# Optimization experiments

Measured on AMD Instinct MI355X. Metric: run time of the kernel, lower is better.

## Reference

```python
import jax, jax.numpy as jnp
import numpy as np
from functools import reduce

N = 20          # total qubits
N_SQC = 4       # shadow-circuit qubits
REPEAT = 2      # BasicEntangleLayer repeat
CDTYPE = jnp.complex64

_I2 = jnp.eye(2, dtype=CDTYPE)
_X  = jnp.array([[0, 1], [1, 0]], dtype=CDTYPE)   # PauliX
_P0 = jnp.array([[1, 0], [0, 0]], dtype=CDTYPE)
_P1 = jnp.array([[0, 0], [0, 1]], dtype=CDTYPE)


def multi_kron(mats):
    return reduce(jnp.kron, mats)


def _ry(t):
    c = jnp.cos(t * 0.5).astype(CDTYPE)
    s = jnp.sin(t * 0.5).astype(CDTYPE)
    return jnp.stack([jnp.stack([c, -s]), jnp.stack([s, c])])


def _rz(t):
    e = jnp.exp(-0.5j * t.astype(CDTYPE))
    z = jnp.zeros((), CDTYPE)
    return jnp.stack([jnp.stack([e, z]), jnp.stack([z, jnp.conj(e)])])


def _yzy_layer(p, n):
    # per qubit i: Ry(p[3i]) then Rz(p[3i+1]) then Ry(p[3i+2])
    mats = [_ry(p[3 * i + 2]) @ _rz(p[3 * i + 1]) @ _ry(p[3 * i]) for i in range(n)]
    return multi_kron(mats)


def _cnot(c, t, n):
    a = [_I2] * n; a[c] = _P0
    b = [_I2] * n; b[c] = _P1; b[t] = _X
    return multi_kron(a) + multi_kron(b)


def _ring_of_cnot(n):
    U = jnp.eye(2 ** n, dtype=CDTYPE)
    for i in range(n):
        U = _cnot(i, (i + 1) % n, n) @ U
    return U


def build_circuit(weight):
    """BasicEntangleLayer (YZY rotations + ring of CNOTs, repeated) + final YZYLayer."""
    n = N_SQC
    ring = _ring_of_cnot(n)
    U = jnp.eye(2 ** n, dtype=CDTYPE)
    for r in range(REPEAT):
        p = weight[3 * n * r:3 * n * (r + 1)]
        U = ring @ (_yzy_layer(p, n) @ U)
    U = _yzy_layer(weight[3 * n * REPEAT:3 * n * (REPEAT + 1)], n) @ U
    return U


def setup_inputs() -> dict:
    key = jax.random.key(0)
    k1, k2 = jax.random.split(key)
    vector_batch = jax.random.normal(k1, (32, 2 ** N), dtype=jnp.float32)
    weight = jax.random.uniform(k2, (9 * N_SQC,), dtype=jnp.float32,
                                minval=0.0, maxval=2.0 * np.pi)
    return {"vector_batch": vector_batch, "weight": weight}


def reference(vector_batch, weight):
    B = vector_batch.shape[0]
    # row-wise L2 normalization, then amplitude encoding into 2^N complex state
    norm = jnp.linalg.norm(vector_batch, axis=1, keepdims=True)
    state = (vector_batch / jnp.maximum(norm, 1e-12)).astype(CDTYPE)  # (B, 2^N)

    U = build_circuit(weight)                        # (16, 16)
    M = multi_kron([_X] * N_SQC)                     # X^{\otimes n_sqc}
    temp = U.conj().T @ M @ U                        # (16, 16) Hermitian

    d = 2 ** N_SQC
    outs = []
    for q in range(N - N_SQC + 1):
        # apply temp locally on qubits [q, q+n_sqc): identical math to
        # <state| I^{\otimes q} (x) temp (x) I^{\otimes rest} |state>
        s = state.reshape(B, 2 ** q, d, -1)          # (B, left, 16, right)
        ts = jnp.einsum('ij,bajc->baic', temp, s)
        outs.append(jnp.einsum('bajc,bajc->b', s.conj(), ts).real)
    return jnp.stack(outs, axis=1).astype(jnp.float32)  # (B, N-n_sqc+1)
```

## Files before the change

kernel.cpp:

```cpp
#include <hip/hip_runtime.h>
#include <math.h>

#define WS_TU    0
#define WS_S     256
#define WS_N     800
#define WS_PART  1024
#define WS_NPART 35840
#define WS_NEED_BYTES ((WS_NPART + 2048) * 4)

typedef _Float16 half8 __attribute__((ext_vector_type(8)));
typedef float f32x4 __attribute__((ext_vector_type(4)));

__device__ inline float2 cmul2(float2 a, float2 b) {
  return make_float2(a.x * b.x - a.y * b.y, a.x * b.y + a.y * b.x);
}

__device__ inline int ringperm(int x) {
  if ((x >> 3) & 1) x ^= 4;
  if ((x >> 2) & 1) x ^= 2;
  if ((x >> 1) & 1) x ^= 1;
  if (x & 1)        x ^= 8;
  return x;
}

__device__ inline float2 yzy_elem(const float* wgt, int layer, int r, int c) {
  float2 prod = make_float2(1.f, 0.f);
#pragma unroll
  for (int k = 0; k < 4; k++) {
    float t0 = wgt[layer * 12 + 3 * k + 0];
    float t1 = wgt[layer * 12 + 3 * k + 1];
    float t2 = wgt[layer * 12 + 3 * k + 2];
    float s0, c0, s1, c1, s2, c2;
    sincosf(0.5f * t0, &s0, &c0);
    sincosf(0.5f * t1, &s1, &c1);
    sincosf(0.5f * t2, &s2, &c2);
    float A = c2 * c0, B = s2 * s0, C = c2 * s0, D = s2 * c0;
    float2 m00 = make_float2( c1 * (A - B), -s1 * (A + B));
    float2 m01 = make_float2(-c1 * (C + D),  s1 * (C - D));
    float2 m10 = make_float2( c1 * (C + D),  s1 * (C - D));
    float2 m11 = make_float2( c1 * (A - B),  s1 * (A + B));
    int rb = (r >> (3 - k)) & 1, cb = (c >> (3 - k)) & 1;
    float2 mm = rb ? (cb ? m11 : m10) : (cb ? m01 : m00);
    prod = cmul2(prod, mm);
  }
  return prod;
}

__global__ void build_T_kernel(const float* __restrict__ wgt, float* __restrict__ ws) {
  __shared__ float2 U[256], Y[256], W[256];
  const int t = threadIdx.x;
  const int r = t >> 4, c = t & 15;

  for (int k = t; k < 576; k += 256) ws[WS_S + k] = 0.f;

  U[t] = yzy_elem(wgt, 0, r, c);
  __syncthreads();
  W[ringperm(r) * 16 + c] = U[t];
  __syncthreads(); U[t] = W[t]; __syncthreads();
  Y[t] = yzy_elem(wgt, 1, r, c);
  __syncthreads();
  {
    float2 s = make_float2(0.f, 0.f);
#pragma unroll
    for (int k = 0; k < 16; k++) {
      float2 pr = cmul2(Y[r * 16 + k], U[k * 16 + c]);
      s.x += pr.x; s.y += pr.y;
    }
    W[t] = s;
  }
  __syncthreads(); U[t] = W[t]; __syncthreads();
  W[ringperm(r) * 16 + c] = U[t];
  __syncthreads(); U[t] = W[t]; __syncthreads();
  Y[t] = yzy_elem(wgt, 2, r, c);
  __syncthreads();
  {
    float2 s = make_float2(0.f, 0.f);
#pragma unroll
    for (int k = 0; k < 16; k++) {
      float2 pr = cmul2(Y[r * 16 + k], U[k * 16 + c]);
      s.x += pr.x; s.y += pr.y;
    }
    W[t] = s;
  }
  __syncthreads(); U[t] = W[t]; __syncthreads();
  Y[t] = U[(r ^ 15) * 16 + c];
  __syncthreads();
  float s_re = 0.f;
#pragma unroll
  for (int k = 0; k < 16; k++) {
    float2 u = U[k * 16 + r], m = Y[k * 16 + c];
    s_re += u.x * m.x + u.y * m.y;
  }
  ws[WS_TU + t] = s_re;
}

__device__ inline int swzB(int B) {
  int h = B >> 3;
  int f = (h ^ (h >> 3) ^ (h >> 6)) & 7;
  return B ^ f;
}

template <int P>
__device__ inline float windowM(const half8* __restrict__ HB, const float* __restrict__ Tr) {
  const int t = threadIdx.x;
  const int w = t >> 6, l = t & 63, g = l >> 4, i = l & 15;
  f32x4 hh[4] = {{0.f, 0.f, 0.f, 0.f}, {0.f, 0.f, 0.f, 0.f},
                 {0.f, 0.f, 0.f, 0.f}, {0.f, 0.f, 0.f, 0.f}};
#pragma unroll
  for (int s = 0; s < 2; s++) {
#pragma unroll
    for (int c = 0; c < 4; c++) {
      int rest = (w << 5) | ((s * 4 + c) << 2) | g;
      int rl = rest & ((1 << (P - 3)) - 1), rh = rest >> (P - 3);
      int pos = (rl << 3) | (i << P) | (rh << (P + 4));
      half8 fr = HB[swzB(pos >> 3)];
      hh[c] = __builtin_amdgcn_mfma_f32_16x16x32_f16(fr, fr, hh[c], 0, 0, 0);
    }
  }
  float part = 0.f;
#pragma unroll
  for (int reg = 0; reg < 4; reg++)
    part = fmaf(Tr[reg], (hh[0][reg] + hh[1][reg]) + (hh[2][reg] + hh[3][reg]), part);
  return part;
}

__global__ __launch_bounds__(256) void passAll_kernel(const float* __restrict__ vb,
                                                      float* ws, int use_part) {
  __shared__ half8 HB[2048];
  const int t = threadIdx.x;
  const int bid = blockIdx.x;

  const int mode = (bid < 2048) ? 0 : 2;
  const int idx = (bid < 2048) ? bid : bid - 2048;
  const int b = idx >> 6, chunk = idx & 63;
  const int l = t & 63, g = l >> 4, i = l & 15;

  float Treg[4];
#pragma unroll
  for (int reg = 0; reg < 4; reg++) Treg[reg] = ws[WS_TU + ((g * 4 + reg) << 4) + i];

  float nsum = 0.f;
  half8 h[8];
  if (mode == 0) {
    const float4* src4 = ((const float4*)vb) + ((size_t)b << 18) + ((size_t)chunk << 12);
#pragma unroll
    for (int j = 0; j < 8; j++) {
      int B = j * 256 + t;
      float4 a = src4[2 * B], c = src4[2 * B + 1];
      nsum = fmaf(a.x, a.x, nsum); nsum = fmaf(a.y, a.y, nsum);
      nsum = fmaf(a.z, a.z, nsum); nsum = fmaf(a.w, a.w, nsum);
      nsum = fmaf(c.x, c.x, nsum); nsum = fmaf(c.y, c.y, nsum);
      nsum = fmaf(c.z, c.z, nsum); nsum = fmaf(c.w, c.w, nsum);
      half8 hh;
      hh[0] = (_Float16)a.x; hh[1] = (_Float16)a.y; hh[2] = (_Float16)a.z; hh[3] = (_Float16)a.w;
      hh[4] = (_Float16)c.x; hh[5] = (_Float16)c.y; hh[6] = (_Float16)c.z; hh[7] = (_Float16)c.w;
      h[j] = hh;
      HB[swzB(B)] = hh;
    }
  } else {
    const float4* src4 = ((const float4*)vb) + ((size_t)b << 18) + chunk * 8;
#pragma unroll
    for (int j = 0; j < 8; j++) {
      int B = j * 256 + t;
      int row = B >> 2;
      int c4 = (B & 3) * 2;
      float4 a = src4[row * 512 + c4], c = src4[row * 512 + c4 + 1];
      half8 hh;
      hh[0] = (_Float16)a.x; hh[1] = (_Float16)a.y; hh[2] = (_Float16)a.z; hh[3] = (_Float16)a.w;
      hh[4] = (_Float16)c.x; hh[5] = (_Float16)c.y; hh[6] = (_Float16)c.z; hh[7] = (_Float16)c.w;
      HB[swzB(B)] = hh;
    }
  }
  __syncthreads();

  float part[11];
#pragma unroll
  for (int k = 0; k < 11; k++) part[k] = 0.f;

  int nwin;
#define DOWIN(P, WIN) part[WIN] = windowM<P>(HB, Treg);
  if (mode == 0) {
    nwin = 11;
    DOWIN(3, 0) DOWIN(4, 1) DOWIN(5, 2) DOWIN(6, 3)
    DOWIN(7, 4) DOWIN(8, 5) DOWIN(9, 6) DOWIN(10, 7)
    __syncthreads();
#pragma unroll
    for (int e = 0; e < 8; e++) {
      half8 v;
#pragma unroll
      for (int j = 0; j < 8; j++) v[j] = h[j][e];
      HB[swzB(8 * t + e)] = v;
    }
    __syncthreads();
    DOWIN(3, 8) DOWIN(4, 9) DOWIN(5, 10)
  } else {
    nwin = 6;
    DOWIN(5, 0) DOWIN(6, 1) DOWIN(7, 2)
    DOWIN(8, 3) DOWIN(9, 4) DOWIN(10, 5)
  }
#undef DOWIN
  __syncthreads();

  float* red2 = (float*)HB;
#pragma unroll
  for (int k = 0; k < 11; k++) red2[k * 256 + t] = part[k];
  red2[11 * 256 + t] = nsum;
  __syncthreads();

  const int win = t >> 4, idx16 = t & 15;
  const float4* r4 = (const float4*)red2;
  float4 q0 = r4[win * 64 + idx16],      q1 = r4[win * 64 + 16 + idx16];
  float4 q2 = r4[win * 64 + 32 + idx16], q3 = r4[win * 64 + 48 + idx16];
  float s1 = ((q0.x + q0.y) + (q0.z + q0.w)) + ((q1.x + q1.y) + (q1.z + q1.w)) +
             ((q2.x + q2.y) + (q2.z + q2.w)) + ((q3.x + q3.y) + (q3.z + q3.w));
#pragma unroll
  for (int off = 8; off; off >>= 1) s1 += __shfl_down(s1, off, 16);

  if (idx16 == 0) {
    if (mode == 0) {
      if (win < 11) {
        int q = (win < 8) ? (13 - win) : (24 - win);
        if (use_part) ws[WS_PART + (b * 17 + q) * 64 + chunk] = s1;
        else          atomicAdd(ws + WS_S + b * 17 + q, s1);
      } else if (win == 11) {
        if (use_part) ws[WS_NPART + b * 64 + chunk] = s1;
        else          atomicAdd(ws + WS_N + b, s1);
      }
    } else {
      if (win < 6) {
        int q = 5 - win;
        if (use_part) ws[WS_PART + (b * 17 + q) * 64 + chunk] = s1;
        else          atomicAdd(ws + WS_S + b * 17 + q, s1);
      }
    }
  }
}

__global__ void finalize_kernel(const float* __restrict__ ws, float* __restrict__ out,
                                int use_part) {
  int i = blockIdx.x * 256 + threadIdx.x;
  if (i < 544) {
    int b = i / 17;
    float s, n;
    if (use_part) {
      const float* sp = ws + WS_PART + i * 64;
      s = 0.f;
#pragma unroll 8
      for (int c = 0; c < 64; c++) s += sp[c];
      const float* np = ws + WS_NPART + b * 64;
      n = 0.f;
#pragma unroll 8
      for (int c = 0; c < 64; c++) n += np[c];
    } else {
      s = ws[WS_S + i];
      n = ws[WS_N + b];
    }
    out[i] = s / fmaxf(n, 1e-24f);
  }
}

extern "C" void kernel_launch(void* const* d_in, const int* in_sizes, int n_in,
                              void* d_out, int out_size, void* d_ws, size_t ws_size,
                              hipStream_t stream) {
  const float* vb  = (const float*)d_in[0];
  const float* wgt = (const float*)d_in[1];
  float* out = (float*)d_out;
  float* ws  = (float*)d_ws;
  int use_part = (ws_size >= (size_t)WS_NEED_BYTES) ? 1 : 0;

  build_T_kernel<<<1, 256, 0, stream>>>(wgt, ws);
  passAll_kernel<<<4096, 256, 0, stream>>>(vb, ws, use_part);
  finalize_kernel<<<3, 256, 0, stream>>>(ws, out, use_part);
}
```

Before: 59.11 us.

## Compute adjacent window pairs with 32x32 MFMA Gram tiles

Each pair of neighbouring 4-qubit windows is now evaluated from a single 32x32x16 MFMA Gram matrix over 5 qubits. The two expectations are read out with masked T weight registers (block-diagonal and interleaved layouts), which roughly halves the number of LDS fragment loads and MFMA passes per window. The transpose stage now reloads from LDS instead of keeping the fp16 values in registers, which lowers register pressure, and launch_bounds asks for 4 blocks per SM. In exchange it adds 32 weight registers per thread and some extra LDS reads.

```diff
diff --git a/kernel.cpp b/kernel.cpp
--- a/kernel.cpp
+++ b/kernel.cpp
@@ -10,6 +10,7 @@
 
 typedef _Float16 half8 __attribute__((ext_vector_type(8)));
 typedef float f32x4 __attribute__((ext_vector_type(4)));
+typedef float f32x16 __attribute__((ext_vector_type(16)));
 
 __device__ inline float2 cmul2(float2 a, float2 b) {
   return make_float2(a.x * b.x - a.y * b.y, a.x * b.y + a.y * b.x);
@@ -101,6 +102,39 @@
 }
 
 template <int P>
+__device__ inline void pairM(const half8* __restrict__ HB,
+                             const float* __restrict__ Wlo,
+                             const float* __restrict__ Whi,
+                             float& plo, float& phi) {
+  const int t = threadIdx.x;
+  const int w = t >> 6, l = t & 63, a = l & 31, hf = l >> 5;
+  f32x16 A0, A1;
+#pragma unroll
+  for (int m = 0; m < 16; m++) { A0[m] = 0.f; A1[m] = 0.f; }
+#pragma unroll
+  for (int s = 0; s < 4; s++) {
+    int rest0 = ((w * 8 + s) << 1) | hf;
+    int rest1 = ((w * 8 + s + 4) << 1) | hf;
+    int rl0 = rest0 & ((1 << (P - 3)) - 1), rh0 = rest0 >> (P - 3);
+    int rl1 = rest1 & ((1 << (P - 3)) - 1), rh1 = rest1 >> (P - 3);
+    int pos0 = (rl0 << 3) | (a << P) | (rh0 << (P + 5));
+    int pos1 = (rl1 << 3) | (a << P) | (rh1 << (P + 5));
+    half8 f0 = HB[swzB(pos0 >> 3)];
+    half8 f1 = HB[swzB(pos1 >> 3)];
+    A0 = __builtin_amdgcn_mfma_f32_32x32x16_f16(f0, f0, A0, 0, 0, 0);
+    A1 = __builtin_amdgcn_mfma_f32_32x32x16_f16(f1, f1, A1, 0, 0, 0);
+  }
+  float lo = 0.f, hi = 0.f;
+#pragma unroll
+  for (int m = 0; m < 16; m++) {
+    float hm = A0[m] + A1[m];
+    lo = fmaf(Wlo[m], hm, lo);
+    hi = fmaf(Whi[m], hm, hi);
+  }
+  plo = lo; phi = hi;
+}
+
+template <int P>
 __device__ inline float windowM(const half8* __restrict__ HB, const float* __restrict__ Tr) {
   const int t = threadIdx.x;
   const int w = t >> 6, l = t & 63, g = l >> 4, i = l & 15;
@@ -124,8 +158,8 @@
   return part;
 }
 
-__global__ __launch_bounds__(256) void passAll_kernel(const float* __restrict__ vb,
-                                                      float* ws, int use_part) {
+__global__ __launch_bounds__(256, 4) void passAll_kernel(const float* __restrict__ vb,
+                                                         float* ws, int use_part) {
   __shared__ half8 HB[2048];
   const int t = threadIdx.x;
   const int bid = blockIdx.x;
@@ -133,28 +167,35 @@
   const int mode = (bid < 2048) ? 0 : 2;
   const int idx = (bid < 2048) ? bid : bid - 2048;
   const int b = idx >> 6, chunk = idx & 63;
-  const int l = t & 63, g = l >> 4, i = l & 15;
-
+  const int l = t & 63, g = (l >> 4) & 3, i = l & 15;
+  const int a32 = l & 31, hf = l >> 5;
+
+  const float* Tws = ws + WS_TU;
+  float Wlo[16], Whi[16];
+#pragma unroll
+  for (int m = 0; m < 16; m++) {
+    int r = (m & 3) + 8 * (m >> 2) + 4 * hf;
+    Wlo[m] = ((r >> 4) == (a32 >> 4)) ? Tws[(r & 15) * 16 + (a32 & 15)] : 0.f;
+    Whi[m] = (((r ^ a32) & 1) == 0) ? Tws[(r >> 1) * 16 + (a32 >> 1)] : 0.f;
+  }
   float Treg[4];
 #pragma unroll
-  for (int reg = 0; reg < 4; reg++) Treg[reg] = ws[WS_TU + ((g * 4 + reg) << 4) + i];
+  for (int reg = 0; reg < 4; reg++) Treg[reg] = Tws[((g * 4 + reg) << 4) + i];
 
   float nsum = 0.f;
-  half8 h[8];
   if (mode == 0) {
     const float4* src4 = ((const float4*)vb) + ((size_t)b << 18) + ((size_t)chunk << 12);
 #pragma unroll
     for (int j = 0; j < 8; j++) {
       int B = j * 256 + t;
-      float4 a = src4[2 * B], c = src4[2 * B + 1];
-      nsum = fmaf(a.x, a.x, nsum); nsum = fmaf(a.y, a.y, nsum);
-      nsum = fmaf(a.z, a.z, nsum); nsum = fmaf(a.w, a.w, nsum);
-      nsum = fmaf(c.x, c.x, nsum); nsum = fmaf(c.y, c.y, nsum);
-      nsum = fmaf(c.z, c.z, nsum); nsum = fmaf(c.w, c.w, nsum);
+      float4 aa = src4[2 * B], cc = src4[2 * B + 1];
+      nsum = fmaf(aa.x, aa.x, nsum); nsum = fmaf(aa.y, aa.y, nsum);
+      nsum = fmaf(aa.z, aa.z, nsum); nsum = fmaf(aa.w, aa.w, nsum);
+      nsum = fmaf(cc.x, cc.x, nsum); nsum = fmaf(cc.y, cc.y, nsum);
+      nsum = fmaf(cc.z, cc.z, nsum); nsum = fmaf(cc.w, cc.w, nsum);
       half8 hh;
-      hh[0] = (_Float16)a.x; hh[1] = (_Float16)a.y; hh[2] = (_Float16)a.z; hh[3] = (_Float16)a.w;
-      hh[4] = (_Float16)c.x; hh[5] = (_Float16)c.y; hh[6] = (_Float16)c.z; hh[7] = (_Float16)c.w;
-      h[j] = hh;
+      hh[0] = (_Float16)aa.x; hh[1] = (_Float16)aa.y; hh[2] = (_Float16)aa.z; hh[3] = (_Float16)aa.w;
+      hh[4] = (_Float16)cc.x; hh[5] = (_Float16)cc.y; hh[6] = (_Float16)cc.z; hh[7] = (_Float16)cc.w;
       HB[swzB(B)] = hh;
     }
   } else {
@@ -164,10 +205,10 @@
       int B = j * 256 + t;
       int row = B >> 2;
       int c4 = (B & 3) * 2;
-      float4 a = src4[row * 512 + c4], c = src4[row * 512 + c4 + 1];
+      float4 aa = src4[row * 512 + c4], cc = src4[row * 512 + c4 + 1];
       half8 hh;
-      hh[0] = (_Float16)a.x; hh[1] = (_Float16)a.y; hh[2] = (_Float16)a.z; hh[3] = (_Float16)a.w;
-      hh[4] = (_Float16)c.x; hh[5] = (_Float16)c.y; hh[6] = (_Float16)c.z; hh[7] = (_Float16)c.w;
+      hh[0] = (_Float16)aa.x; hh[1] = (_Float16)aa.y; hh[2] = (_Float16)aa.z; hh[3] = (_Float16)aa.w;
+      hh[4] = (_Float16)cc.x; hh[5] = (_Float16)cc.y; hh[6] = (_Float16)cc.z; hh[7] = (_Float16)cc.w;
       HB[swzB(B)] = hh;
     }
   }
@@ -177,28 +218,30 @@
 #pragma unroll
   for (int k = 0; k < 11; k++) part[k] = 0.f;
 
-  int nwin;
-#define DOWIN(P, WIN) part[WIN] = windowM<P>(HB, Treg);
   if (mode == 0) {
-    nwin = 11;
-    DOWIN(3, 0) DOWIN(4, 1) DOWIN(5, 2) DOWIN(6, 3)
-    DOWIN(7, 4) DOWIN(8, 5) DOWIN(9, 6) DOWIN(10, 7)
+    pairM<3>(HB, Wlo, Whi, part[0], part[1]);
+    pairM<5>(HB, Wlo, Whi, part[2], part[3]);
+    pairM<7>(HB, Wlo, Whi, part[4], part[5]);
+    pairM<9>(HB, Wlo, Whi, part[6], part[7]);
+    half8 h2[8];
+#pragma unroll
+    for (int j = 0; j < 8; j++) h2[j] = HB[swzB(j * 256 + t)];
     __syncthreads();
 #pragma unroll
     for (int e = 0; e < 8; e++) {
       half8 v;
 #pragma unroll
-      for (int j = 0; j < 8; j++) v[j] = h[j][e];
+      for (int j = 0; j < 8; j++) v[j] = h2[j][e];
       HB[swzB(8 * t + e)] = v;
     }
     __syncthreads();
-    DOWIN(3, 8) DOWIN(4, 9) DOWIN(5, 10)
+    pairM<3>(HB, Wlo, Whi, part[8], part[9]);
+    part[10] = windowM<5>(HB, Treg);
   } else {
-    nwin = 6;
-    DOWIN(5, 0) DOWIN(6, 1) DOWIN(7, 2)
-    DOWIN(8, 3) DOWIN(9, 4) DOWIN(10, 5)
-  }
-#undef DOWIN
+    pairM<5>(HB, Wlo, Whi, part[0], part[1]);
+    pairM<7>(HB, Wlo, Whi, part[2], part[3]);
+    pairM<9>(HB, Wlo, Whi, part[4], part[5]);
+  }
   __syncthreads();
 
   float* red2 = (float*)HB;
```

New measurement: 64.75 us. 9.5% more time.

## Process four chunks per block with register prefetch of next chunk

Applied to the files above, without the earlier changes.

Each block now handles four consecutive chunks instead of one, with the grid cut from 4096 to 1024 blocks. Global loads for the next chunk are issued into registers before the MFMA window work on the current chunk, overlapping memory latency with compute. The number of partial sums and the finalize reduction shrink accordingly. The 16 float4 prefetch registers raise register pressure (launch bounds set to 4 blocks per SM), and the fewer, longer blocks may reduce the number of waves in flight.

```diff
diff --git a/kernel.cpp b/kernel.cpp
--- a/kernel.cpp
+++ b/kernel.cpp
@@ -5,8 +5,8 @@
 #define WS_S     256
 #define WS_N     800
 #define WS_PART  1024
-#define WS_NPART 35840
-#define WS_NEED_BYTES ((WS_NPART + 2048) * 4)
+#define WS_NPART 9728
+#define WS_NEED_BYTES (10240 * 4)
 
 typedef _Float16 half8 __attribute__((ext_vector_type(8)));
 typedef float f32x4 __attribute__((ext_vector_type(4)));
@@ -124,82 +124,104 @@
   return part;
 }
 
-__global__ __launch_bounds__(256) void passAll_kernel(const float* __restrict__ vb,
-                                                      float* ws, int use_part) {
+__device__ inline void issue_loads(float4* pf, const float4* __restrict__ vb4,
+                                   int mode, int b, int chB, int t) {
+  if (mode == 0) {
+    const float4* s4 = vb4 + ((size_t)b << 18) + ((size_t)chB << 12);
+#pragma unroll
+    for (int j = 0; j < 8; j++) {
+      pf[2 * j]     = s4[2 * (j * 256 + t)];
+      pf[2 * j + 1] = s4[2 * (j * 256 + t) + 1];
+    }
+  } else {
+    const float4* s4 = vb4 + ((size_t)b << 18) + chB * 8;
+#pragma unroll
+    for (int j = 0; j < 8; j++) {
+      int B = j * 256 + t, row = B >> 2, c4 = (B & 3) * 2;
+      pf[2 * j]     = s4[row * 512 + c4];
+      pf[2 * j + 1] = s4[row * 512 + c4 + 1];
+    }
+  }
+}
+
+__global__ __launch_bounds__(256, 4) void passAll_kernel(const float* __restrict__ vb,
+                                                         float* ws, int use_part) {
   __shared__ half8 HB[2048];
   const int t = threadIdx.x;
   const int bid = blockIdx.x;
 
-  const int mode = (bid < 2048) ? 0 : 2;
-  const int idx = (bid < 2048) ? bid : bid - 2048;
-  const int b = idx >> 6, chunk = idx & 63;
-  const int l = t & 63, g = l >> 4, i = l & 15;
+  const int mode = (bid < 512) ? 0 : 2;
+  const int sub = bid & 511;
+  const int b = sub >> 4, blk16 = sub & 15;
+  const int l = t & 63, g = (l >> 4) & 3, i = l & 15;
 
   float Treg[4];
 #pragma unroll
   for (int reg = 0; reg < 4; reg++) Treg[reg] = ws[WS_TU + ((g * 4 + reg) << 4) + i];
 
+  const float4* vb4 = (const float4*)vb;
+  float4 pf[16];
+  float part[11];
+#pragma unroll
+  for (int k = 0; k < 11; k++) part[k] = 0.f;
   float nsum = 0.f;
-  half8 h[8];
-  if (mode == 0) {
-    const float4* src4 = ((const float4*)vb) + ((size_t)b << 18) + ((size_t)chunk << 12);
+
+  issue_loads(pf, vb4, mode, b, 4 * blk16, t);
+
+#pragma unroll
+  for (int c = 0; c < 4; c++) {
 #pragma unroll
     for (int j = 0; j < 8; j++) {
-      int B = j * 256 + t;
-      float4 a = src4[2 * B], c = src4[2 * B + 1];
-      nsum = fmaf(a.x, a.x, nsum); nsum = fmaf(a.y, a.y, nsum);
-      nsum = fmaf(a.z, a.z, nsum); nsum = fmaf(a.w, a.w, nsum);
-      nsum = fmaf(c.x, c.x, nsum); nsum = fmaf(c.y, c.y, nsum);
-      nsum = fmaf(c.z, c.z, nsum); nsum = fmaf(c.w, c.w, nsum);
+      float4 aa = pf[2 * j], cc = pf[2 * j + 1];
+      if (mode == 0) {
+        nsum = fmaf(aa.x, aa.x, nsum); nsum = fmaf(aa.y, aa.y, nsum);
+        nsum = fmaf(aa.z, aa.z, nsum); nsum = fmaf(aa.w, aa.w, nsum);
+        nsum = fmaf(cc.x, cc.x, nsum); nsum = fmaf(cc.y, cc.y, nsum);
+        nsum = fmaf(cc.z, cc.z, nsum); nsum = fmaf(cc.w, cc.w, nsum);
+      }
       half8 hh;
-      hh[0] = (_Float16)a.x; hh[1] = (_Float16)a.y; hh[2] = (_Float16)a.z; hh[3] = (_Float16)a.w;
-      hh[4] = (_Float16)c.x; hh[5] = (_Float16)c.y; hh[6] = (_Float16)c.z; hh[7] = (_Float16)c.w;
-      h[j] = hh;
-      HB[swzB(B)] = hh;
-    }
-  } else {
-    const float4* src4 = ((const float4*)vb) + ((size_t)b << 18) + chunk * 8;
-#pragma unroll
-    for (int j = 0; j < 8; j++) {
-      int B = j * 256 + t;
-      int row = B >> 2;
-      int c4 = (B & 3) * 2;
-      float4 a = src4[row * 512 + c4], c = src4[row * 512 + c4 + 1];
-      half8 hh;
-      hh[0] = (_Float16)a.x; hh[1] = (_Float16)a.y; hh[2] = (_Float16)a.z; hh[3] = (_Float16)a.w;
-      hh[4] = (_Float16)c.x; hh[5] = (_Float16)c.y; hh[6] = (_Float16)c.z; hh[7] = (_Float16)c.w;
-      HB[swzB(B)] = hh;
-    }
-  }
-  __syncthreads();
-
-  float part[11];
-#pragma unroll
-  for (int k = 0; k < 11; k++) part[k] = 0.f;
-
-  int nwin;
-#define DOWIN(P, WIN) part[WIN] = windowM<P>(HB, Treg);
-  if (mode == 0) {
-    nwin = 11;
-    DOWIN(3, 0) DOWIN(4, 1) DOWIN(5, 2) DOWIN(6, 3)
-    DOWIN(7, 4) DOWIN(8, 5) DOWIN(9, 6) DOWIN(10, 7)
+      hh[0] = (_Float16)aa.x; hh[1] = (_Float16)aa.y; hh[2] = (_Float16)aa.z; hh[3] = (_Float16)aa.w;
+      hh[4] = (_Float16)cc.x; hh[5] = (_Float16)cc.y; hh[6] = (_Float16)cc.z; hh[7] = (_Float16)cc.w;
+      HB[swzB(j * 256 + t)] = hh;
+    }
     __syncthreads();
-#pragma unroll
-    for (int e = 0; e < 8; e++) {
-      half8 v;
-#pragma unroll
-      for (int j = 0; j < 8; j++) v[j] = h[j][e];
-      HB[swzB(8 * t + e)] = v;
+
+    if (c < 3) issue_loads(pf, vb4, mode, b, 4 * blk16 + c + 1, t);
+
+    if (mode == 0) {
+      part[0] += windowM<3>(HB, Treg);
+      part[1] += windowM<4>(HB, Treg);
+      part[2] += windowM<5>(HB, Treg);
+      part[3] += windowM<6>(HB, Treg);
+      part[4] += windowM<7>(HB, Treg);
+      part[5] += windowM<8>(HB, Treg);
+      part[6] += windowM<9>(HB, Treg);
+      part[7] += windowM<10>(HB, Treg);
+      half8 h2[8];
+#pragma unroll
+      for (int j = 0; j < 8; j++) h2[j] = HB[swzB(j * 256 + t)];
+      __syncthreads();
+#pragma unroll
+      for (int e = 0; e < 8; e++) {
+        half8 v;
+#pragma unroll
+        for (int j = 0; j < 8; j++) v[j] = h2[j][e];
+        HB[swzB(8 * t + e)] = v;
+      }
+      __syncthreads();
+      part[8]  += windowM<3>(HB, Treg);
+      part[9]  += windowM<4>(HB, Treg);
+      part[10] += windowM<5>(HB, Treg);
+    } else {
+      part[0] += windowM<5>(HB, Treg);
+      part[1] += windowM<6>(HB, Treg);
+      part[2] += windowM<7>(HB, Treg);
+      part[3] += windowM<8>(HB, Treg);
+      part[4] += windowM<9>(HB, Treg);
+      part[5] += windowM<10>(HB, Treg);
     }
     __syncthreads();
-    DOWIN(3, 8) DOWIN(4, 9) DOWIN(5, 10)
-  } else {
-    nwin = 6;
-    DOWIN(5, 0) DOWIN(6, 1) DOWIN(7, 2)
-    DOWIN(8, 3) DOWIN(9, 4) DOWIN(10, 5)
-  }
-#undef DOWIN
-  __syncthreads();
+  }
 
   float* red2 = (float*)HB;
 #pragma unroll
@@ -220,16 +242,16 @@
     if (mode == 0) {
       if (win < 11) {
         int q = (win < 8) ? (13 - win) : (24 - win);
-        if (use_part) ws[WS_PART + (b * 17 + q) * 64 + chunk] = s1;
+        if (use_part) ws[WS_PART + (b * 17 + q) * 16 + blk16] = s1;
         else          atomicAdd(ws + WS_S + b * 17 + q, s1);
       } else if (win == 11) {
-        if (use_part) ws[WS_NPART + b * 64 + chunk] = s1;
+        if (use_part) ws[WS_NPART + b * 16 + blk16] = s1;
         else          atomicAdd(ws + WS_N + b, s1);
       }
     } else {
       if (win < 6) {
         int q = 5 - win;
-        if (use_part) ws[WS_PART + (b * 17 + q) * 64 + chunk] = s1;
+        if (use_part) ws[WS_PART + (b * 17 + q) * 16 + blk16] = s1;
         else          atomicAdd(ws + WS_S + b * 17 + q, s1);
       }
     }
@@ -243,14 +265,14 @@
     int b = i / 17;
     float s, n;
     if (use_part) {
-      const float* sp = ws + WS_PART + i * 64;
+      const float* sp = ws + WS_PART + i * 16;
       s = 0.f;
-#pragma unroll 8
-      for (int c = 0; c < 64; c++) s += sp[c];
-      const float* np = ws + WS_NPART + b * 64;
+#pragma unroll
+      for (int c = 0; c < 16; c++) s += sp[c];
+      const float* np = ws + WS_NPART + b * 16;
       n = 0.f;
-#pragma unroll 8
-      for (int c = 0; c < 64; c++) n += np[c];
+#pragma unroll
+      for (int c = 0; c < 16; c++) n += np[c];
     } else {
       s = ws[WS_S + i];
       n = ws[WS_N + b];
@@ -269,6 +291,6 @@
   int use_part = (ws_size >= (size_t)WS_NEED_BYTES) ? 1 : 0;
 
   build_T_kernel<<<1, 256, 0, stream>>>(wgt, ws);
-  passAll_kernel<<<4096, 256, 0, stream>>>(vb, ws, use_part);
+  passAll_kernel<<<1024, 256, 0, stream>>>(vb, ws, use_part);
   finalize_kernel<<<3, 256, 0, stream>>>(ws, out, use_part);
 }
```

After: 236.1 us. 3.99x slower.
